# Performance work log

Measured on AMD Instinct MI355X. Metric: run time of the kernel, lower is better.

Reference implementation:

```python
import jax, jax.numpy as jnp
import numpy as np

EPS = 1e-5
NUM_HEADS = 16
HEAD_DIM = 128


def setup_inputs() -> dict:
    key = jax.random.key(0)
    ks = jax.random.split(key, 9)
    B, S, D = 2, 2048, 2048
    Hd2 = HEAD_DIM // 2
    # rotary angles: proper cos/sin of random phases (unit-modulus freqs_cis)
    theta = jax.random.uniform(ks[1], (B, S, Hd2), jnp.float32, 0.0, 2 * np.pi)
    return {
        "hidden_states": jax.random.normal(ks[0], (B, S, D), jnp.float32),
        "freqs_cos": jnp.cos(theta),
        "freqs_sin": jnp.sin(theta),
        "Wq": jax.random.normal(ks[2], (D, D), jnp.float32) * (D ** -0.5),
        "Wk": jax.random.normal(ks[3], (D, D), jnp.float32) * (D ** -0.5),
        "Wv": jax.random.normal(ks[4], (D, D), jnp.float32) * (D ** -0.5),
        "Wo": jax.random.normal(ks[5], (D, D), jnp.float32) * (D ** -0.5),
        "gq": jnp.ones((HEAD_DIM,), jnp.float32),
        "gk": jnp.ones((HEAD_DIM,), jnp.float32),
    }


def _rmsnorm(x, g):
    # normalize over last (head) dim, eps=1e-5, learned scale
    var = jnp.mean(jnp.square(x), axis=-1, keepdims=True)
    return x * jax.lax.rsqrt(var + EPS) * g


def _rope(x, cos, sin):
    # x: [B,S,H,hd]; treat last dim as hd/2 complex pairs; cos/sin: [B,S,hd/2]
    B, S, H, hd = x.shape
    xp = x.reshape(B, S, H, hd // 2, 2)
    xr, xi = xp[..., 0], xp[..., 1]
    c = cos[:, :, None, :]
    s = sin[:, :, None, :]
    out_r = xr * c - xi * s
    out_i = xr * s + xi * c
    return jnp.stack([out_r, out_i], axis=-1).reshape(B, S, H, hd)


def reference(hidden_states, freqs_cos, freqs_sin, Wq, Wk, Wv, Wo, gq, gk):
    B, S, D = hidden_states.shape
    H, hd = NUM_HEADS, HEAD_DIM
    q = (hidden_states @ Wq).reshape(B, S, H, hd)
    k = (hidden_states @ Wk).reshape(B, S, H, hd)
    v = (hidden_states @ Wv).reshape(B, S, H, hd)
    q = _rmsnorm(q, gq)
    k = _rmsnorm(k, gk)
    q = _rope(q, freqs_cos, freqs_sin)
    k = _rope(k, freqs_cos, freqs_sin)
    scale = 1.0 / np.sqrt(hd)
    scores = jnp.einsum("bqhd,bkhd->bhqk", q, k) * scale
    attn = jax.nn.softmax(scores, axis=-1)
    out = jnp.einsum("bhqk,bkhd->bqhd", attn, v)  # [B,S,H,hd]
    out = out.reshape(B, S, H * hd)
    return out @ Wo
```

## Files before the change

### kernel.cpp

```cpp
#include <hip/hip_runtime.h>
#include <hip/hip_bf16.h>

typedef __attribute__((ext_vector_type(8))) short bf16x8;
typedef __attribute__((ext_vector_type(4))) short bf16x4;
typedef __attribute__((ext_vector_type(4))) float f32x4;
typedef __attribute__((ext_vector_type(16))) float f32x16;
typedef __attribute__((ext_vector_type(4))) int   i32x4;
typedef __attribute__((ext_vector_type(2))) unsigned u32x2;
typedef __attribute__((ext_vector_type(4))) unsigned u32x4;

#define D_MODEL 2048
#define NTOK    4096
#define NH      16
#define HD      128
#define SEQ     2048
#define NQKV    6144

__device__ __forceinline__ short f2bf(float f) {
  unsigned u = __builtin_bit_cast(unsigned, f);
  unsigned r = u + 0x7FFFu + ((u >> 16) & 1u);
  return (short)(r >> 16);
}
__device__ __forceinline__ float bf2f(short s) {
  return __builtin_bit_cast(float, ((unsigned)(unsigned short)s) << 16);
}

__device__ __forceinline__ float exp2fast(float x) {
#if __has_builtin(__builtin_amdgcn_exp2f)
  return __builtin_amdgcn_exp2f(x);
#else
  return exp2f(x);
#endif
}

__device__ __forceinline__ unsigned cvt_pk_bf16(float a, float b) {
  unsigned r;
  asm("v_cvt_pk_bf16_f32 %0, %1, %2" : "=v"(r) : "v"(a), "v"(b));
  return r;
}

__device__ __forceinline__ void permswap(unsigned& x, unsigned& y) {
#if __has_builtin(__builtin_amdgcn_permlane32_swap)
  u32x2 r = __builtin_amdgcn_permlane32_swap(x, y, false, false);
  x = r[0]; y = r[1];
#else
  asm volatile("v_permlane32_swap_b32 %0, %1" : "+v"(x), "+v"(y));
#endif
}

__device__ __forceinline__ f32x16 mfma32(bf16x8 a, bf16x8 b, f32x16 c) {
  return __builtin_amdgcn_mfma_f32_32x32x16_bf16(a, b, c, 0, 0, 0);
}

__device__ __forceinline__ void gload_lds16(const void* g, void* l) {
  typedef __attribute__((address_space(1))) const unsigned gu32;
  typedef __attribute__((address_space(3))) unsigned lu32;
  __builtin_amdgcn_global_load_lds((gu32*)(uintptr_t)g,
                                   (lu32*)(unsigned)(uintptr_t)l, 16, 0, 0);
}

__global__ __launch_bounds__(256) void cast_bf16(const float* __restrict__ in,
                                                 short* __restrict__ out, int n4) {
  int i = blockIdx.x * 256 + threadIdx.x;
  if (i >= n4) return;
  float4 v = ((const float4*)in)[i];
  short4 o;
  o.x = f2bf(v.x); o.y = f2bf(v.y); o.z = f2bf(v.z); o.w = f2bf(v.w);
  ((short4*)out)[i] = o;
}

__global__ __launch_bounds__(256) void wtrans(const float* __restrict__ w0,
                                              const float* __restrict__ w1,
                                              const float* __restrict__ w2,
                                              const float* __restrict__ w3,
                                              short* __restrict__ wt) {
  int z = blockIdx.z;
  const float* W = (z == 0) ? w0 : (z == 1) ? w1 : (z == 2) ? w2 : w3;
  short* O = wt + (size_t)z * D_MODEL * D_MODEL;
  int n0 = blockIdx.x * 64, k0 = blockIdx.y * 64;
  __shared__ short T[64 * 136];
  int tid = threadIdx.x;
#pragma unroll
  for (int it = 0; it < 4; ++it) {
    int f = it * 256 + tid, kk = f >> 4, nc = f & 15;
    float4 v = *(const float4*)&W[(size_t)(k0 + kk) * D_MODEL + n0 + nc * 4];
    short4 o;
    o.x = f2bf(v.x); o.y = f2bf(v.y); o.z = f2bf(v.z); o.w = f2bf(v.w);
    *(short4*)&T[kk * 136 + nc * 4] = o;
  }
  __syncthreads();
#pragma unroll
  for (int it = 0; it < 4; ++it) {
    int u = it * 256 + tid, nn = u >> 4, kc = u & 15;
    short4 o;
    o.x = T[(kc * 4 + 0) * 136 + nn];
    o.y = T[(kc * 4 + 1) * 136 + nn];
    o.z = T[(kc * 4 + 2) * 136 + nn];
    o.w = T[(kc * 4 + 3) * 136 + nn];
    *(short4*)&O[(size_t)(n0 + nn) * D_MODEL + k0 + kc * 4] = o;
  }
}

template <bool OUTBF16>
__global__ __launch_bounds__(512, 2) void gemm8(const short* __restrict__ A,
                                                const short* __restrict__ Bt,
                                                void* __restrict__ Cv, int CS) {
  __shared__ short L[4 * 12288];
  int tid = threadIdx.x, w = tid >> 6, lane = tid & 63, c = lane & 15, g = lane >> 4;

  int gx = gridDim.x, gy = gridDim.y;
  int lin = blockIdx.x + gx * blockIdx.y;
  int idx = lin >> 3, nst = (gx * gy) >> 7;
  int s = (lin & 7) * nst + (idx >> 4);
  int w16 = idx & 15;
  int smR = gy >> 2;
  int mblk = (s % smR) * 4 + (w16 >> 2);
  int nblk = (s / smR) * 4 + (w16 & 3);
  int m0 = mblk * 256, n0 = nblk * 128;
  int wm = w >> 1, wn = w & 1;

  const int NKT = D_MODEL / 32;

  int asrc[2], bsrc;
#pragma unroll
  for (int q = 0; q < 2; ++q) {
    int o = (2 * w + q) * 1024 + lane * 16;
    int os = o ^ (((o >> 7) & 7) << 4);
    asrc[q] = (m0 + (os >> 6)) * D_MODEL + ((os & 63) >> 1);
  }
  {
    int o = w * 1024 + lane * 16;
    int os = o ^ (((o >> 7) & 7) << 4);
    bsrc = (n0 + (os >> 6)) * D_MODEL + ((os & 63) >> 1);
  }

  int aoff[4], boff[4];
#pragma unroll
  for (int mi = 0; mi < 4; ++mi) {
    int r = wm * 64 + mi * 16 + c;
    int o = r * 64 + g * 16;
    aoff[mi] = o ^ (((o >> 7) & 7) << 4);
  }
#pragma unroll
  for (int ni = 0; ni < 4; ++ni) {
    int r = wn * 64 + ni * 16 + c;
    int o = r * 64 + g * 16;
    boff[ni] = 16384 + (o ^ (((o >> 7) & 7) << 4));
  }

  auto STAGE = [&](int jt) {
    int kk = jt * 32;
    char* base = (char*)L + (jt & 3) * 24576;
    gload_lds16(A + asrc[0] + kk, base + (2 * w) * 1024);
    gload_lds16(A + asrc[1] + kk, base + (2 * w + 1) * 1024);
    gload_lds16(Bt + bsrc + kk, base + 16384 + w * 1024);
  };

  f32x4 acc[4][4] = {};

  STAGE(0); STAGE(1); STAGE(2);
  asm volatile("s_waitcnt vmcnt(6)" ::: "memory");
  __builtin_amdgcn_s_barrier();
  asm volatile("" ::: "memory");

  for (int jt = 0; jt < NKT; ++jt) {
    if (jt + 3 < NKT) STAGE(jt + 3);
    const char* buf = (const char*)L + (jt & 3) * 24576;
    bf16x8 af[4], bfv[4];
#pragma unroll
    for (int mi = 0; mi < 4; ++mi) af[mi] = *(const bf16x8*)(buf + aoff[mi]);
#pragma unroll
    for (int ni = 0; ni < 4; ++ni) bfv[ni] = *(const bf16x8*)(buf + boff[ni]);
    __builtin_amdgcn_s_setprio(1);
#pragma unroll
    for (int mi = 0; mi < 4; ++mi)
#pragma unroll
      for (int ni = 0; ni < 4; ++ni)
        acc[mi][ni] = __builtin_amdgcn_mfma_f32_16x16x32_bf16(af[mi], bfv[ni],
                                                              acc[mi][ni], 0, 0, 0);
    __builtin_amdgcn_s_setprio(0);
    if (jt + 1 < NKT) {
      if (jt + 3 <= NKT - 1)      { asm volatile("s_waitcnt vmcnt(6)" ::: "memory"); }
      else if (jt + 2 <= NKT - 1) { asm volatile("s_waitcnt vmcnt(3)" ::: "memory"); }
      else                        { asm volatile("s_waitcnt vmcnt(0)" ::: "memory"); }
      __builtin_amdgcn_s_barrier();
      asm volatile("" ::: "memory");
    }
  }

  int row0 = m0 + wm * 64, col0 = n0 + wn * 64;
  if (OUTBF16) {
    short* Cb = (short*)Cv;
#pragma unroll
    for (int mi = 0; mi < 4; ++mi)
#pragma unroll
      for (int ni = 0; ni < 4; ++ni)
#pragma unroll
        for (int i = 0; i < 4; ++i)
          Cb[(size_t)(row0 + mi * 16 + g * 4 + i) * CS + col0 + ni * 16 + c] =
              f2bf(acc[mi][ni][i]);
  } else {
    float* Cf = (float*)Cv;
#pragma unroll
    for (int mi = 0; mi < 4; ++mi)
#pragma unroll
      for (int ni = 0; ni < 4; ++ni)
#pragma unroll
        for (int i = 0; i < 4; ++i)
          Cf[(size_t)(row0 + mi * 16 + g * 4 + i) * CS + col0 + ni * 16 + c] =
              acc[mi][ni][i];
  }
}

__global__ __launch_bounds__(256) void norm_rope(const short* __restrict__ qkv16,
                                                 const float* __restrict__ cosb,
                                                 const float* __restrict__ sinb,
                                                 const float* __restrict__ gq,
                                                 const float* __restrict__ gk,
                                                 short* __restrict__ qn,
                                                 short* __restrict__ kn) {
  int z = blockIdx.y;
  const float* gg = z ? gk : gq;
  short* O = z ? kn : qn;
  int w = threadIdx.x >> 6, lane = threadIdx.x & 63;
  int p = blockIdx.x * 4 + w;
  int token = p >> 4, h = p & 15;
  int v = *(const int*)&qkv16[(size_t)token * NQKV + z * D_MODEL + h * HD + lane * 2];
  float x0 = bf2f((short)(v & 0xffff));
  float x1 = bf2f((short)((unsigned)v >> 16));
  float ss = x0 * x0 + x1 * x1;
#pragma unroll
  for (int mk = 32; mk; mk >>= 1) ss += __shfl_xor(ss, mk);
  float rs = rsqrtf(ss * (1.f / 128.f) + 1e-5f);
  float qs = z ? 1.0f : 0.12751744f;
  rs *= qs;
  float xr = x0 * rs * gg[lane * 2];
  float xi = x1 * rs * gg[lane * 2 + 1];
  float cc = cosb[(size_t)token * 64 + lane];
  float sn = sinb[(size_t)token * 64 + lane];
  float or_ = xr * cc - xi * sn;
  float oi_ = xr * sn + xi * cc;
  int b = token >> 11, sidx = token & 2047;
  size_t dst = ((size_t)(b * NH + h) * SEQ + sidx) * HD + lane * 2;
  unsigned pk = (unsigned)(unsigned short)f2bf(or_) |
                ((unsigned)(unsigned short)f2bf(oi_) << 16);
  *(unsigned*)&O[dst] = pk;
}

__global__ __launch_bounds__(256) void vtrans(const short* __restrict__ qkv16,
                                              short* __restrict__ vt) {
  int st = blockIdx.x, bh = blockIdx.y;
  int b = bh >> 4, h = bh & 15;
  int t0 = b * SEQ + st * 64;
  __shared__ short Lt[64 * 136];
  int tid = threadIdx.x;
#pragma unroll
  for (int it = 0; it < 4; ++it) {
    int f = it * 256 + tid, tk = f >> 4, ch = f & 15;
    *(i32x4*)&Lt[tk * 136 + ch * 8] =
        *(const i32x4*)&qkv16[(size_t)(t0 + tk) * NQKV + 2 * D_MODEL + h * HD + ch * 8];
  }
  __syncthreads();
#pragma unroll
  for (int it = 0; it < 4; ++it) {
    int u = it * 256 + tid, d = u >> 3, kg = u & 7;
    bf16x8 o;
#pragma unroll
    for (int j = 0; j < 8; ++j) o[j] = Lt[(kg * 8 + j) * 136 + d];
    *(bf16x8*)&vt[(size_t)(bh * HD + d) * SEQ + st * 64 + kg * 8] = o;
  }
}

__global__ __launch_bounds__(512, 2) void flash(const short* __restrict__ qn,
                                                const short* __restrict__ kn,
                                                const short* __restrict__ vt,
                                                short* __restrict__ attn) {
  __shared__ short Ks[2][64 * 128];
  __shared__ short Vs[2][128 * 64];
  int tid = threadIdx.x, w = tid >> 6, lane = tid & 63;
  int q31 = lane & 31, hi = lane >> 5;

  int phys = blockIdx.x;
  int xcd = phys & 7, idx = phys >> 3;
  int bh = xcd * 4 + (idx >> 3);
  int qb = idx & 7;
  int q0 = qb * 256 + w * 32;

  const size_t base = (size_t)bh * SEQ * HD;
  const short* Kg = kn + base;
  const short* Vg = vt + base;

  bf16x8 qf[8];
#pragma unroll
  for (int s = 0; s < 8; ++s)
    qf[s] = *(const bf16x8*)&qn[base + (size_t)(q0 + q31) * HD + s * 16 + hi * 8];

  f32x16 acc[4] = {};
  float m_ = -1e30f, l_ = 0.f;

  int ksrc[2], vsrc[2];
#pragma unroll
  for (int p = 0; p < 2; ++p) {
    int ch = w * 2 + p;
    int o = ch * 1024 + lane * 16;
    int kr = o >> 8, kc = o & 255;
    ksrc[p] = kr * HD + ((kc ^ ((kr & 7) << 4)) >> 1);
    int vr = o >> 7, vc = o & 127;
    vsrc[p] = vr * SEQ + ((vc ^ ((vr & 7) << 4)) >> 1);
  }
  int swz = (q31 & 7) << 4;
  int koff[8], voff[4];
#pragma unroll
  for (int kf = 0; kf < 8; ++kf) koff[kf] = (kf * 32 + hi * 16) ^ swz;
#pragma unroll
  for (int kk = 0; kk < 4; ++kk) voff[kk] = (kk * 32 + hi * 16) ^ swz;
  int krow0 = q31 * 256, krow1 = (32 + q31) * 256;

#pragma unroll
  for (int p = 0; p < 2; ++p) {
    int ch = w * 2 + p;
    gload_lds16(Kg + ksrc[p], (char*)&Ks[0][0] + ch * 1024);
    gload_lds16(Vg + vsrc[p], (char*)&Vs[0][0] + ch * 1024);
  }

  const int NT = SEQ / 64;
  for (int t = 0; t < NT; ++t) {
    int cur = t & 1;
    __syncthreads();
    if (t + 1 < NT) {
      int k0n = (t + 1) * 64;
#pragma unroll
      for (int p = 0; p < 2; ++p) {
        int ch = w * 2 + p;
        gload_lds16(Kg + (size_t)k0n * HD + ksrc[p], (char*)&Ks[cur ^ 1][0] + ch * 1024);
        gload_lds16(Vg + k0n + vsrc[p],              (char*)&Vs[cur ^ 1][0] + ch * 1024);
      }
    }
    const char* Kb = (const char*)&Ks[cur][0];
    const char* Vb = (const char*)&Vs[cur][0];

    f32x16 s0 = {0,0,0,0,0,0,0,0,0,0,0,0,0,0,0,0};
    f32x16 s1 = {0,0,0,0,0,0,0,0,0,0,0,0,0,0,0,0};
    __builtin_amdgcn_s_setprio(1);
#pragma unroll
    for (int kf = 0; kf < 8; ++kf) {
      bf16x8 k0 = *(const bf16x8*)(Kb + krow0 + koff[kf]);
      s0 = mfma32(k0, qf[kf], s0);
      bf16x8 k1 = *(const bf16x8*)(Kb + krow1 + koff[kf]);
      s1 = mfma32(k1, qf[kf], s1);
    }
    __builtin_amdgcn_s_setprio(0);

    float p0 = -1e30f, p1 = -1e30f, p2 = -1e30f, p3 = -1e30f;
#pragma unroll
    for (int i = 0; i < 4; ++i) {
      p0 = fmaxf(p0, fmaxf(s0[i], s0[i + 4]));
      p1 = fmaxf(p1, fmaxf(s0[i + 8], s0[i + 12]));
      p2 = fmaxf(p2, fmaxf(s1[i], s1[i + 4]));
      p3 = fmaxf(p3, fmaxf(s1[i + 8], s1[i + 12]));
    }
    float pmax = fmaxf(fmaxf(p0, p1), fmaxf(p2, p3));
    pmax = fmaxf(pmax, __shfl_xor(pmax, 32));
    if (!__all(pmax <= m_ + 11.5f)) {
      float mn = fmaxf(m_, pmax);
      float al = exp2fast(m_ - mn);
      m_ = mn; l_ *= al;
#pragma unroll
      for (int db = 0; db < 4; ++db)
#pragma unroll
        for (int i = 0; i < 16; ++i) acc[db][i] *= al;
    }
    float r0 = 0.f, r1 = 0.f;
#pragma unroll
    for (int i = 0; i < 16; ++i) {
      float pa = exp2fast(s0[i] - m_); r0 += pa; s0[i] = pa;
      float pb = exp2fast(s1[i] - m_); r1 += pb; s1[i] = pb;
    }
    float r = r0 + r1;
    r += __shfl_xor(r, 32);
    l_ += r;

    __builtin_amdgcn_s_setprio(1);
#pragma unroll
    for (int kt = 0; kt < 2; ++kt) {
      const f32x16& sv = kt ? s1 : s0;
#pragma unroll
      for (int c2 = 0; c2 < 2; ++c2) {
        unsigned x0 = cvt_pk_bf16(sv[c2 * 8 + 0], sv[c2 * 8 + 1]);
        unsigned x1 = cvt_pk_bf16(sv[c2 * 8 + 2], sv[c2 * 8 + 3]);
        unsigned y0 = cvt_pk_bf16(sv[c2 * 8 + 4], sv[c2 * 8 + 5]);
        unsigned y1 = cvt_pk_bf16(sv[c2 * 8 + 6], sv[c2 * 8 + 7]);
        permswap(x0, y0);
        permswap(x1, y1);
        u32x4 pw = {x0, x1, y0, y1};
        bf16x8 pfrag = __builtin_bit_cast(bf16x8, pw);
        int vo = voff[kt * 2 + c2];
#pragma unroll
        for (int db = 0; db < 4; ++db) {
          bf16x8 va = *(const bf16x8*)(Vb + (db * 32 + q31) * 128 + vo);
          acc[db] = mfma32(va, pfrag, acc[db]);
        }
      }
    }
    __builtin_amdgcn_s_setprio(0);
  }

  int b = bh >> 4, h = bh & 15;
  float linv = 1.f / l_;
  size_t orow = (size_t)(b * SEQ + q0 + q31) * D_MODEL + h * HD;
#pragma unroll
  for (int db = 0; db < 4; ++db)
#pragma unroll
    for (int rg = 0; rg < 4; ++rg) {
      short4 o;
      o.x = f2bf(acc[db][rg * 4 + 0] * linv);
      o.y = f2bf(acc[db][rg * 4 + 1] * linv);
      o.z = f2bf(acc[db][rg * 4 + 2] * linv);
      o.w = f2bf(acc[db][rg * 4 + 3] * linv);
      *(short4*)&attn[orow + db * 32 + rg * 8 + hi * 4] = o;
    }
}

extern "C" void kernel_launch(void* const* d_in, const int* in_sizes, int n_in,
                              void* d_out, int out_size, void* d_ws, size_t ws_size,
                              hipStream_t stream) {
  const float* hs   = (const float*)d_in[0];
  const float* fcos = (const float*)d_in[1];
  const float* fsin = (const float*)d_in[2];
  const float* Wq   = (const float*)d_in[3];
  const float* Wk   = (const float*)d_in[4];
  const float* Wv   = (const float*)d_in[5];
  const float* Wo   = (const float*)d_in[6];
  const float* gq   = (const float*)d_in[7];
  const float* gk   = (const float*)d_in[8];

  char* ws = (char*)d_ws;
  short* hs16  = (short*)ws;
  short* Wt    = (short*)(ws + 16777216);
  short* qkv16 = (short*)(ws + 50331648);
  short* qn    = (short*)(ws + 100663296);
  short* kn    = (short*)(ws + 117440512);
  short* vt    = (short*)(ws + 134217728);
  short* attn16 = hs16;

  cast_bf16<<<8192, 256, 0, stream>>>(hs, hs16, NTOK * D_MODEL / 4);
  wtrans<<<dim3(32, 32, 4), 256, 0, stream>>>(Wq, Wk, Wv, Wo, Wt);
  gemm8<true><<<dim3(48, 16), 512, 0, stream>>>(hs16, Wt, qkv16, NQKV);
  norm_rope<<<dim3(16384, 2), 256, 0, stream>>>(qkv16, fcos, fsin, gq, gk, qn, kn);
  vtrans<<<dim3(32, 32), 256, 0, stream>>>(qkv16, vt);
  flash<<<dim3(256), 512, 0, stream>>>(qn, kn, vt, attn16);
  gemm8<false><<<dim3(16, 16), 512, 0, stream>>>(attn16,
                                                 Wt + (size_t)3 * D_MODEL * D_MODEL,
                                                 d_out, D_MODEL);
}
```

Measured before the change: 283.1 us.

## Double GEMM K-tile to 64 with 3-stage LDS ring and interleaved loads

Restructures the bf16 GEMM main loop to use a K-tile of 64 instead of 32. The LDS ring drops from 4 stages to 3, and each K-tile is split into two MFMA phases, each issuing half of the next-stage global-to-LDS loads. This halves the number of main-loop iterations and their barrier/waitcnt overhead, and spreads the memory traffic across the compute. In exchange, LDS use per block grows from 96KB to 144KB, which can limit occupancy, and each phase adds a barrier.

```diff
diff --git a/kernel.cpp b/kernel.cpp
--- a/kernel.cpp
+++ b/kernel.cpp
@@ -102,10 +102,10 @@
 }
 
 template <bool OUTBF16>
-__global__ __launch_bounds__(512, 2) void gemm8(const short* __restrict__ A,
-                                                const short* __restrict__ Bt,
-                                                void* __restrict__ Cv, int CS) {
-  __shared__ short L[4 * 12288];
+__global__ __launch_bounds__(512, 2) void gemm8p(const short* __restrict__ A,
+                                                 const short* __restrict__ Bt,
+                                                 void* __restrict__ Cv, int CS) {
+  __shared__ char L[3 * 49152];
   int tid = threadIdx.x, w = tid >> 6, lane = tid & 63, c = lane & 15, g = lane >> 4;
 
   int gx = gridDim.x, gy = gridDim.y;
@@ -119,72 +119,79 @@
   int m0 = mblk * 256, n0 = nblk * 128;
   int wm = w >> 1, wn = w & 1;
 
-  const int NKT = D_MODEL / 32;
-
-  int asrc[2], bsrc;
-#pragma unroll
-  for (int q = 0; q < 2; ++q) {
-    int o = (2 * w + q) * 1024 + lane * 16;
-    int os = o ^ (((o >> 7) & 7) << 4);
-    asrc[q] = (m0 + (os >> 6)) * D_MODEL + ((os & 63) >> 1);
-  }
-  {
-    int o = w * 1024 + lane * 16;
-    int os = o ^ (((o >> 7) & 7) << 4);
-    bsrc = (n0 + (os >> 6)) * D_MODEL + ((os & 63) >> 1);
-  }
-
-  int aoff[4], boff[4];
-#pragma unroll
-  for (int mi = 0; mi < 4; ++mi) {
-    int r = wm * 64 + mi * 16 + c;
-    int o = r * 64 + g * 16;
-    aoff[mi] = o ^ (((o >> 7) & 7) << 4);
-  }
-#pragma unroll
-  for (int ni = 0; ni < 4; ++ni) {
-    int r = wn * 64 + ni * 16 + c;
-    int o = r * 64 + g * 16;
-    boff[ni] = 16384 + (o ^ (((o >> 7) & 7) << 4));
-  }
-
-  auto STAGE = [&](int jt) {
-    int kk = jt * 32;
-    char* base = (char*)L + (jt & 3) * 24576;
-    gload_lds16(A + asrc[0] + kk, base + (2 * w) * 1024);
-    gload_lds16(A + asrc[1] + kk, base + (2 * w + 1) * 1024);
-    gload_lds16(Bt + bsrc + kk, base + 16384 + w * 1024);
-  };
+  const int NKT = D_MODEL / 64;
+
+  const short* gsrc[6];
+  int ldst[6];
+#pragma unroll
+  for (int j = 0; j < 6; ++j) {
+    int ch = (j / 3) * 24 + w * 3 + (j % 3);
+    int o = (ch < 32 ? ch * 1024 : (ch - 32) * 1024) + lane * 16;
+    int r = o >> 7, colb = o & 127;
+    int sw = (colb ^ ((r & 7) << 4)) >> 1;
+    gsrc[j] = (ch < 32) ? A + (size_t)(m0 + r) * D_MODEL + sw
+                        : Bt + (size_t)(n0 + r) * D_MODEL + sw;
+    ldst[j] = ch * 1024;
+  }
+
+  int aoff[2][4], boff[2][4];
+#pragma unroll
+  for (int ks = 0; ks < 2; ++ks) {
+#pragma unroll
+    for (int mi = 0; mi < 4; ++mi) {
+      int r = wm * 64 + mi * 16 + c;
+      aoff[ks][mi] = r * 128 + ((ks * 64 + g * 16) ^ ((r & 7) << 4));
+    }
+#pragma unroll
+    for (int ni = 0; ni < 4; ++ni) {
+      int r = wn * 64 + ni * 16 + c;
+      boff[ks][ni] = 32768 + r * 128 + ((ks * 64 + g * 16) ^ ((r & 7) << 4));
+    }
+  }
 
   f32x4 acc[4][4] = {};
 
-  STAGE(0); STAGE(1); STAGE(2);
+#pragma unroll
+  for (int j = 0; j < 6; ++j) gload_lds16(gsrc[j], L + ldst[j]);
+#pragma unroll
+  for (int j = 0; j < 6; ++j) gload_lds16(gsrc[j] + 64, L + 49152 + ldst[j]);
   asm volatile("s_waitcnt vmcnt(6)" ::: "memory");
   __builtin_amdgcn_s_barrier();
-  asm volatile("" ::: "memory");
-
-  for (int jt = 0; jt < NKT; ++jt) {
-    if (jt + 3 < NKT) STAGE(jt + 3);
-    const char* buf = (const char*)L + (jt & 3) * 24576;
-    bf16x8 af[4], bfv[4];
-#pragma unroll
-    for (int mi = 0; mi < 4; ++mi) af[mi] = *(const bf16x8*)(buf + aoff[mi]);
-#pragma unroll
-    for (int ni = 0; ni < 4; ++ni) bfv[ni] = *(const bf16x8*)(buf + boff[ni]);
-    __builtin_amdgcn_s_setprio(1);
-#pragma unroll
-    for (int mi = 0; mi < 4; ++mi)
-#pragma unroll
-      for (int ni = 0; ni < 4; ++ni)
-        acc[mi][ni] = __builtin_amdgcn_mfma_f32_16x16x32_bf16(af[mi], bfv[ni],
-                                                              acc[mi][ni], 0, 0, 0);
-    __builtin_amdgcn_s_setprio(0);
-    if (jt + 1 < NKT) {
-      if (jt + 3 <= NKT - 1)      { asm volatile("s_waitcnt vmcnt(6)" ::: "memory"); }
-      else if (jt + 2 <= NKT - 1) { asm volatile("s_waitcnt vmcnt(3)" ::: "memory"); }
-      else                        { asm volatile("s_waitcnt vmcnt(0)" ::: "memory"); }
+
+  for (int kt = 0; kt < NKT; ++kt) {
+    const char* buf = L + (kt % 3) * 49152;
+    char* sbase = L + ((kt + 2) % 3) * 49152;
+    int skk = (kt + 2) * 64;
+    bool dostage = (kt + 2 < NKT);
+#pragma unroll
+    for (int ph = 0; ph < 2; ++ph) {
+      bf16x8 af[4], bfv[4];
+#pragma unroll
+      for (int mi = 0; mi < 4; ++mi) af[mi] = *(const bf16x8*)(buf + aoff[ph][mi]);
+#pragma unroll
+      for (int ni = 0; ni < 4; ++ni) bfv[ni] = *(const bf16x8*)(buf + boff[ph][ni]);
+      if (dostage) {
+#pragma unroll
+        for (int j = ph * 3; j < ph * 3 + 3; ++j)
+          gload_lds16(gsrc[j] + skk, sbase + ldst[j]);
+      }
+      __builtin_amdgcn_sched_barrier(0);
       __builtin_amdgcn_s_barrier();
-      asm volatile("" ::: "memory");
+      asm volatile("s_waitcnt lgkmcnt(0)" ::: "memory");
+      __builtin_amdgcn_sched_barrier(0);
+      __builtin_amdgcn_s_setprio(1);
+#pragma unroll
+      for (int mi = 0; mi < 4; ++mi)
+#pragma unroll
+        for (int ni = 0; ni < 4; ++ni)
+          acc[mi][ni] = __builtin_amdgcn_mfma_f32_16x16x32_bf16(af[mi], bfv[ni],
+                                                                acc[mi][ni], 0, 0, 0);
+      __builtin_amdgcn_s_setprio(0);
+      if (ph == 1) {
+        if (kt + 2 < NKT)      { asm volatile("s_waitcnt vmcnt(6)" ::: "memory"); }
+        else if (kt + 1 < NKT) { asm volatile("s_waitcnt vmcnt(0)" ::: "memory"); }
+      }
+      __builtin_amdgcn_s_barrier();
     }
   }
 
@@ -445,11 +452,11 @@
 
   cast_bf16<<<8192, 256, 0, stream>>>(hs, hs16, NTOK * D_MODEL / 4);
   wtrans<<<dim3(32, 32, 4), 256, 0, stream>>>(Wq, Wk, Wv, Wo, Wt);
-  gemm8<true><<<dim3(48, 16), 512, 0, stream>>>(hs16, Wt, qkv16, NQKV);
+  gemm8p<true><<<dim3(48, 16), 512, 0, stream>>>(hs16, Wt, qkv16, NQKV);
   norm_rope<<<dim3(16384, 2), 256, 0, stream>>>(qkv16, fcos, fsin, gq, gk, qn, kn);
   vtrans<<<dim3(32, 32), 256, 0, stream>>>(qkv16, vt);
   flash<<<dim3(256), 512, 0, stream>>>(qn, kn, vt, attn16);
-  gemm8<false><<<dim3(16, 16), 512, 0, stream>>>(attn16,
-                                                 Wt + (size_t)3 * D_MODEL * D_MODEL,
-                                                 d_out, D_MODEL);
-}
+  gemm8p<false><<<dim3(16, 16), 512, 0, stream>>>(attn16,
+                                                  Wt + (size_t)3 * D_MODEL * D_MODEL,
+                                                  d_out, D_MODEL);
+}
```

New measurement: 273.8 us. 3.3% less time.
